# Performance work log

Hardware: AMD Instinct MI355X
Metric: run time of the kernel (lower is better)

Reference implementation:

```python
import jax, jax.numpy as jnp
import numpy as np
from jax import lax

B, T, DIN = 512, 96, 64
H = 256          # hidden_dim
P = 2            # patch_size
L = 4            # n_layers
HEADS = 8
E = 3 * H        # encoder_dim = hidden_dim * len(scales)
NC = 100         # num_classes
EPS = 1e-5


def layernorm(x, g, b):
    m = x.mean(-1, keepdims=True)
    v = ((x - m) ** 2).mean(-1, keepdims=True)
    return (x - m) * lax.rsqrt(v + EPS) * g + b


def conv1d(x, w, b, k):
    # x: [B, C, T], w: [O, I, k]; torch padding='same' (extra pad on the right for even k)
    lo = (k - 1) // 2
    hi = (k - 1) - lo
    y = lax.conv_general_dilated(x, w, (1,), [(lo, hi)],
                                 dimension_numbers=('NCH', 'OIH', 'NCH'))
    return y + b[None, :, None]


def fourier_attn(x, Wqkv, Wo, bo):
    Bx, Tx, Ex = x.shape
    dh = Ex // HEADS
    qkv = x @ Wqkv                                   # [B,T,3E]
    q, k, v = jnp.split(qkv, 3, axis=-1)
    to_heads = lambda t: t.reshape(Bx, Tx, HEADS, dh).transpose(0, 2, 1, 3)  # [B,h,T,dh]
    q, k, v = to_heads(q), to_heads(k), to_heads(v)
    qf = jnp.fft.rfft(q, axis=-2)
    kf = jnp.fft.rfft(k, axis=-2)
    attn = jnp.sum(jnp.conj(qf) * kf, axis=-1).real * (dh ** -0.5)  # [B,h,F]
    attn = jax.nn.softmax(attn, axis=-1)
    vf = jnp.fft.rfft(v, axis=-2)                    # [B,h,F,dh]
    out = jnp.fft.irfft(attn[..., None] * vf, n=Tx, axis=-2)        # [B,h,T,dh]
    out = out.transpose(0, 2, 1, 3).reshape(Bx, Tx, Ex)
    return out @ Wo + bo


def setup_inputs() -> dict:
    key = jax.random.key(0)
    ks = iter(jax.random.split(key, 40))
    nrm = lambda shape, s=0.02: jax.random.normal(next(ks), shape, jnp.float32) * s
    z = lambda *shape: jnp.zeros(shape, jnp.float32)
    o = lambda *shape: jnp.ones(shape, jnp.float32)
    return dict(
        x=jax.random.normal(next(ks), (B, T, DIN), jnp.float32),
        W_in=nrm((DIN, H)), b_in=z(H),
        pe=nrm((1, 100, H)),
        W_shape=nrm((H, H)), b_shape=z(H),
        W_patch=nrm((P * H, H)), b_patch=z(H),
        conv_w1=nrm((H, H, 1)), conv_b1=z(H),
        conv_w2=nrm((H, H, 2)), conv_b2=z(H),
        conv_w4=nrm((H, H, 4)), conv_b4=z(H),
        ln1_g=o(L, E), ln1_b=z(L, E),
        Wqkv=nrm((L, E, 3 * E)),
        Wo=nrm((L, E, E)), bo=z(L, E),
        ln2_g=o(L, E), ln2_b=z(L, E),
        Wf1=nrm((L, E, 4 * E)), bf1=z(L, 4 * E),
        Wf2=nrm((L, 4 * E, E)), bf2=z(L, E),
        ssm_w=nrm((E, E, 3)), ssm_b=z(E),
        ssm_g=o(E), ssm_bn=z(E),
        W_out=nrm((E, NC)), b_out=z(NC),
    )


def reference(x, W_in, b_in, pe, W_shape, b_shape, W_patch, b_patch,
              conv_w1, conv_b1, conv_w2, conv_b2, conv_w4, conv_b4,
              ln1_g, ln1_b, Wqkv, Wo, bo, ln2_g, ln2_b, Wf1, bf1, Wf2, bf2,
              ssm_w, ssm_b, ssm_g, ssm_bn, W_out, b_out):
    h = x @ W_in + b_in                              # [B,T,H]
    h = h + pe[:, :h.shape[1], :]
    # shape-aware embedding: diff with prepend of first step
    sf = jnp.diff(h, axis=1, prepend=h[:, :1, :])
    h = h + sf @ W_shape + b_shape
    # patch embedding: [B,T,H] -> [B,T/P,P*H] -> [B,T/P,H]
    Bx, Tx, Dx = h.shape
    h = h.reshape(Bx, Tx // P, P * Dx) @ W_patch + b_patch
    # multiscale fourier: rfft.real then 3 same-padded convs, concat channels
    f = jnp.fft.rfft(h, axis=1).real                 # [B,F,H], F = T/P//2 + 1
    fc = f.transpose(0, 2, 1)                        # [B,H,F]
    m1 = conv1d(fc, conv_w1, conv_b1, 1).transpose(0, 2, 1)
    m2 = conv1d(fc, conv_w2, conv_b2, 2).transpose(0, 2, 1)
    m4 = conv1d(fc, conv_w4, conv_b4, 4).transpose(0, 2, 1)
    h = jnp.concatenate([m1, m2, m4], axis=-1)       # [B,F,E]
    for i in range(L):
        h = h + fourier_attn(layernorm(h, ln1_g[i], ln1_b[i]), Wqkv[i], Wo[i], bo[i])
        y = layernorm(h, ln2_g[i], ln2_b[i])
        y = jax.nn.gelu(y @ Wf1[i] + bf1[i], approximate=False) @ Wf2[i] + bf2[i]
        h = h + y
    # simple SSM: depth conv residual + layernorm
    s = conv1d(h.transpose(0, 2, 1), ssm_w, ssm_b, 3).transpose(0, 2, 1)
    h = layernorm(h + s, ssm_g, ssm_bn)
    return h.mean(axis=1) @ W_out + b_out            # [B,NC]
```

## Files before the change

kernel.cpp:

```cpp
#include <hip/hip_runtime.h>
#include <hip/hip_bf16.h>
#include <math.h>

#define Bsz 512
#define Tin 96
#define DIN 64
#define Hd  256
#define Pp  2
#define Ll  4
#define NHEAD 8
#define Ed  768
#define NCls 100
#define Tp  48
#define Ff  25
#define F2  13
#define DH  96

#define E_BIAS 1
#define E_PE   2
#define E_RES  4
#define E_ACC  8
#define E_GELU 16
#define E_OUTS 32
#define E_SPLK 64

typedef unsigned short ushortT;
typedef unsigned short ushort8 __attribute__((ext_vector_type(8)));
typedef short short8 __attribute__((ext_vector_type(8)));
typedef float f32x4 __attribute__((ext_vector_type(4)));

static __device__ __forceinline__ ushortT f2bf(float f) {
  __hip_bfloat16 h = __float2bfloat16(f);
  return *reinterpret_cast<ushortT*>(&h);
}
static __device__ __forceinline__ float bfbits2f(ushortT u) {
  unsigned int x = ((unsigned int)u) << 16;
  return __uint_as_float(x);
}
static __device__ __forceinline__ void split2(float v, ushortT& h, ushortT& l) {
  h = f2bf(v);
  l = f2bf(v - bfbits2f(h));
}

typedef const __attribute__((address_space(1))) void* gas1_t;
typedef __attribute__((address_space(3))) void* las3_t;
static __device__ __forceinline__ void gload16(const void* g, void* l) {
  __builtin_amdgcn_global_load_lds((gas1_t)g, (las3_t)l, 16, 0, 0);
}

constexpr int GBM = 128, GBN = 128, GBK = 32;

template<int AMODE, int ASRC, int EPI>
__global__ __launch_bounds__(256) void gemm3(
    const float* __restrict__ A,
    const ushortT* __restrict__ Ah, const ushortT* __restrict__ Al,
    const ushortT* __restrict__ Bh, const ushortT* __restrict__ Bl,
    const float* __restrict__ bias, const float* __restrict__ extra,
    float* __restrict__ C, ushortT* __restrict__ Coh, ushortT* __restrict__ Col,
    int M, int N, int K, int Ald, int Tdim, int lo, int Kin, int Cld, int coff,
    int Mt, int Nt, int mmaj, int ksn)
{
  __shared__ __align__(16) ushortT Ash[GBM * GBK];
  __shared__ __align__(16) ushortT Asl[GBM * GBK];
  __shared__ __align__(16) ushortT Bsh[GBN * GBK];
  __shared__ __align__(16) ushortT Bsl[GBN * GBK];
  int tid = threadIdx.x;

  int lin = blockIdx.x;
  int G = gridDim.x;
  int r8 = lin & 7, s8 = lin >> 3;
  int q = G >> 3, rem = G & 7;
  int start = r8 * q + (r8 < rem ? r8 : rem);
  int idx = start + s8;
  int tiles = Mt * Nt;
  int ks = 0;
  if (ksn > 1) { ks = idx / tiles; idx -= ks * tiles; }
  int mt, nt;
  if (mmaj) { mt = idx / Nt; nt = idx - mt * Nt; }
  else      { nt = idx / Mt; mt = idx - nt * Mt; }
  int m0 = mt * GBM, n0 = nt * GBN;
  int kper = K / ksn;
  int kbeg = ks * kper, kend = kbeg + kper;

  int wid = tid >> 6, lane = tid & 63;
  int wm = wid & 1, wn = wid >> 1;
  int m16 = lane & 15, quad = lane >> 4;

  f32x4 acc[4][4] = {};

  int grow = (wid << 5) + (lane >> 2);
  int gcb  = (lane & 3) << 4;
  int scb  = gcb ^ (((grow >> 1) & 3) << 4);
  char* ldsA = (char*)Ash + (wid << 11);
  char* ldsa = (char*)Asl + (wid << 11);
  char* ldsB = (char*)Bsh + (wid << 11);
  char* ldsb = (char*)Bsl + (wid << 11);
  size_t bo0 = ((size_t)(n0 + grow) * K) * 2 + scb;
  size_t bo1 = bo0 + (size_t)(16 * K) * 2;
  size_t ao0 = 0, ao1 = 0;
  if (ASRC == 1) {
    int ar0 = m0 + grow;       if (ar0 >= M) ar0 = M - 1;
    int ar1 = m0 + grow + 16;  if (ar1 >= M) ar1 = M - 1;
    ao0 = ((size_t)ar0 * Ald) * 2 + scb;
    ao1 = ((size_t)ar1 * Ald) * 2 + scb;
  }

  int srow = tid >> 1;
  int skh  = (tid & 1) << 4;
  int sswz = ((srow >> 1) & 3) << 3;
  int st0 = srow * GBK + (skh ^ sswz);
  int st1 = srow * GBK + ((skh + 8) ^ sswz);

  int fswz = ((m16 >> 1) & 3) << 3;
  int scf  = (quad << 3) ^ fswz;

  for (int k0 = kbeg; k0 < kend; k0 += GBK) {
    size_t kb = (size_t)k0 * 2;
    gload16((const char*)Bh + bo0 + kb, ldsB);
    gload16((const char*)Bh + bo1 + kb, ldsB + 1024);
    gload16((const char*)Bl + bo0 + kb, ldsb);
    gload16((const char*)Bl + bo1 + kb, ldsb + 1024);
    if (ASRC == 1) {
      gload16((const char*)Ah + ao0 + kb, ldsA);
      gload16((const char*)Ah + ao1 + kb, ldsA + 1024);
      gload16((const char*)Al + ao0 + kb, ldsa);
      gload16((const char*)Al + ao1 + kb, ldsa + 1024);
    } else {
      int row = m0 + srow;
      if (row >= M) row = M - 1;
      float tf[16];
      if (AMODE == 0) {
        const float* p = A + (size_t)row * Ald + k0 + skh;
#pragma unroll
        for (int j = 0; j < 16; j += 4) {
          float4 v = *(const float4*)(p + j);
          tf[j] = v.x; tf[j+1] = v.y; tf[j+2] = v.z; tf[j+3] = v.w;
        }
      } else if (AMODE == 1) {
        int t = row % Tdim;
        const float* p = A + (size_t)row * Ald + k0 + skh;
#pragma unroll
        for (int j = 0; j < 16; j += 4) {
          float4 v = *(const float4*)(p + j);
          float4 w = (t != 0) ? *(const float4*)(p - Ald + j) : v;
          tf[j] = v.x - w.x; tf[j+1] = v.y - w.y;
          tf[j+2] = v.z - w.z; tf[j+3] = v.w - w.w;
        }
      } else {
        int kk = k0 + skh;
        int tap = kk / Kin;
        int i0  = kk - tap * Kin;
        int bb = row / Tdim;
        int t  = row - bb * Tdim;
        int tt = t - lo + tap;
        if (tt >= 0 && tt < Tdim) {
          const float* p = A + ((size_t)bb * Tdim + tt) * Ald + i0;
#pragma unroll
          for (int j = 0; j < 16; j += 4) {
            float4 v = *(const float4*)(p + j);
            tf[j] = v.x; tf[j+1] = v.y; tf[j+2] = v.z; tf[j+3] = v.w;
          }
        } else {
#pragma unroll
          for (int j = 0; j < 16; j++) tf[j] = 0.0f;
        }
      }
      ushortT th[16], tl[16];
#pragma unroll
      for (int j = 0; j < 16; j++) split2(tf[j], th[j], tl[j]);
      *(ushort8*)&Ash[st0] = *(ushort8*)&th[0];
      *(ushort8*)&Ash[st1] = *(ushort8*)&th[8];
      *(ushort8*)&Asl[st0] = *(ushort8*)&tl[0];
      *(ushort8*)&Asl[st1] = *(ushort8*)&tl[8];
    }
    __syncthreads();
    short8 ah[4], al[4], bh[4], bl[4];
#pragma unroll
    for (int i = 0; i < 4; i++) {
      int ro = (wm * 64 + i * 16 + m16) * GBK + scf;
      ah[i] = *(short8*)&Ash[ro];
      al[i] = *(short8*)&Asl[ro];
    }
#pragma unroll
    for (int j = 0; j < 4; j++) {
      int ro = (wn * 64 + j * 16 + m16) * GBK + scf;
      bh[j] = *(short8*)&Bsh[ro];
      bl[j] = *(short8*)&Bsl[ro];
    }
#pragma unroll
    for (int i = 0; i < 4; i++)
#pragma unroll
      for (int j = 0; j < 4; j++) {
        acc[i][j] = __builtin_amdgcn_mfma_f32_16x16x32_bf16(ah[i], bh[j], acc[i][j], 0, 0, 0);
        acc[i][j] = __builtin_amdgcn_mfma_f32_16x16x32_bf16(al[i], bh[j], acc[i][j], 0, 0, 0);
        acc[i][j] = __builtin_amdgcn_mfma_f32_16x16x32_bf16(ah[i], bl[j], acc[i][j], 0, 0, 0);
      }
    __syncthreads();
  }

#pragma unroll
  for (int i = 0; i < 4; i++) {
#pragma unroll
    for (int j = 0; j < 4; j++) {
      int colg = n0 + wn * 64 + j * 16 + m16;
#pragma unroll
      for (int rr = 0; rr < 4; rr++) {
        int rowg = m0 + wm * 64 + i * 16 + quad * 4 + rr;
        if (rowg >= M) continue;
        float v = acc[i][j][rr];
        if ((EPI & E_BIAS) && ks == 0) v += bias[colg];
        if (EPI & E_PE)   v += extra[(size_t)(rowg % Tdim) * N + colg];
        if (EPI & E_RES)  v += extra[(size_t)rowg * Cld + colg];
        if (EPI & E_GELU) v = 0.5f * v * (1.0f + erff(v * 0.70710678118654752f));
        size_t off = (size_t)rowg * Cld + coff + colg;
        if (EPI & E_SPLK) {
          atomicAdd(&C[off], v);
        } else if (EPI & E_OUTS) {
          ushortT h, l; split2(v, h, l);
          Coh[off] = h; Col[off] = l;
        } else {
          if (EPI & E_ACC) v += C[off];
          C[off] = v;
        }
      }
    }
  }
}

#define GEMM3(AM, AS, EP, KS, Asrc, AhP, AlP, BhP, BlP, biasP, extraP, CP, CohP, ColP, \
              Mv, Nv, Kv, AldV, TdimV, loV, KinV, CldV, coffV) \
  do { int Mt_ = (Mv) / GBM, Nt_ = (Nv) / GBN; int mm_ = ((Mv) >= (Nv)) ? 1 : 0; \
       gemm3<AM, AS, EP><<<dim3(Mt_ * Nt_ * (KS)), dim3(256), 0, stream>>>( \
           Asrc, AhP, AlP, BhP, BlP, biasP, extraP, CP, CohP, ColP, \
           Mv, Nv, Kv, AldV, TdimV, loV, KinV, CldV, coffV, Mt_, Nt_, mm_, KS); } while (0)

__global__ __launch_bounds__(256) void wcvt_t_split(
    const float* __restrict__ W, ushortT* __restrict__ Wh, ushortT* __restrict__ Wl,
    int K, int N)
{
  __shared__ float t[32][33];
  int k0 = blockIdx.y * 32, n0 = blockIdx.x * 32;
  int tx = threadIdx.x;
  int ty = threadIdx.y;
#pragma unroll
  for (int dy = 0; dy < 32; dy += 8)
    t[ty + dy][tx] = W[(size_t)(k0 + ty + dy) * N + n0 + tx];
  __syncthreads();
#pragma unroll
  for (int dy = 0; dy < 32; dy += 8) {
    float v = t[tx][ty + dy];
    ushortT h, l;
    split2(v, h, l);
    size_t off = (size_t)(n0 + ty + dy) * K + k0 + tx;
    Wh[off] = h; Wl[off] = l;
  }
}

__global__ __launch_bounds__(256) void wcvt_split(
    const float* __restrict__ W, ushortT* __restrict__ Wh, ushortT* __restrict__ Wl, int n)
{
  int gid = blockIdx.x * 256 + threadIdx.x;
  int stride = gridDim.x * 256;
  for (int i = gid; i < n; i += stride) {
    ushortT h, l;
    split2(W[i], h, l);
    Wh[i] = h; Wl[i] = l;
  }
}

__global__ __launch_bounds__(256) void wcvt_split_tm(
    const float* __restrict__ W, ushortT* __restrict__ Wh, ushortT* __restrict__ Wl,
    int O, int Kin, int NT)
{
  int n = O * Kin * NT;
  int gid = blockIdx.x * 256 + threadIdx.x;
  int stride = gridDim.x * 256;
  for (int idx = gid; idx < n; idx += stride) {
    int o = idx / (Kin * NT);
    int rr = idx - o * (Kin * NT);
    int tap = rr / Kin;
    int i = rr - tap * Kin;
    float v = W[(size_t)o * Kin * NT + (size_t)i * NT + tap];
    ushortT h, l;
    split2(v, h, l);
    Wh[idx] = h; Wl[idx] = l;
  }
}

constexpr int BM = 64, BN = 64, BK = 16, TM = 4, TN = 4;
__global__ __launch_bounds__(256) void gemm_cls(
    const float* __restrict__ A, const float* __restrict__ Bw,
    const float* __restrict__ bias, float* __restrict__ C,
    int M, int N, int K, int Ald, int Cld)
{
  __shared__ alignas(16) float As[BK][BM + 4];
  __shared__ alignas(16) float Bs[BK][BN + 4];
  int tid = threadIdx.x;
  int n0 = blockIdx.x * BN;
  int m0 = blockIdx.y * BM;
  int tx = tid & 15, ty = tid >> 4;
  float acc[TM][TN];
#pragma unroll
  for (int i = 0; i < TM; i++)
#pragma unroll
    for (int j = 0; j < TN; j++) acc[i][j] = 0.0f;
  int a_m = tid >> 2, a_k = (tid & 3) * 4;
  int b_k = tid >> 4, b_n = (tid & 15) * 4;
  for (int k0 = 0; k0 < K; k0 += BK) {
    int row = m0 + a_m;
#pragma unroll
    for (int j = 0; j < 4; j++)
      As[a_k + j][a_m] = A[(size_t)row * Ald + k0 + a_k + j];
    int kk = k0 + b_k;
#pragma unroll
    for (int j = 0; j < 4; j++) {
      int nn = n0 + b_n + j;
      Bs[b_k][b_n + j] = (nn < N) ? Bw[(size_t)kk * N + nn] : 0.0f;
    }
    __syncthreads();
#pragma unroll
    for (int k = 0; k < BK; k++) {
      float4 av = *reinterpret_cast<const float4*>(&As[k][ty * TM]);
      float4 bv = *reinterpret_cast<const float4*>(&Bs[k][tx * TN]);
      float a4[4] = {av.x, av.y, av.z, av.w};
      float b4[4] = {bv.x, bv.y, bv.z, bv.w};
#pragma unroll
      for (int i = 0; i < TM; i++)
#pragma unroll
        for (int j = 0; j < TN; j++) acc[i][j] += a4[i] * b4[j];
    }
    __syncthreads();
  }
#pragma unroll
  for (int i = 0; i < TM; i++) {
    int row = m0 + ty * TM + i;
#pragma unroll
    for (int j = 0; j < TN; j++) {
      int col = n0 + tx * TN + j;
      if (col >= N) continue;
      C[(size_t)row * Cld + col] = acc[i][j] + bias[col];
    }
  }
}

__global__ __launch_bounds__(256) void rfft48_kernel(
    const float* __restrict__ hp, float* __restrict__ f)
{
  int kf = blockIdx.x;
  int b  = blockIdx.y;
  int tid = threadIdx.x;
  __shared__ float ct[48];
  if (tid < 48) {
    int rr = (kf * tid) % 48;
    ct[tid] = cosf(6.2831853071795864f * (float)rr / 48.0f);
  }
  __syncthreads();
  const float* hb = hp + (size_t)b * Tp * Hd;
  float s = 0.0f;
  for (int t = 0; t < 48; t++) s += hb[t * Hd + tid] * ct[t];
  f[((size_t)b * Ff + kf) * Hd + tid] = s;
}

__global__ __launch_bounds__(256) void attn_fused(
    const float* __restrict__ qkv,
    ushortT* __restrict__ oh, ushortT* __restrict__ ol)
{
  int bh = blockIdx.x;
  int b = bh >> 3, h = bh & 7;
  __shared__ float qs[Ff * DH], ks[Ff * DH], vs[Ff * DH];
  __shared__ float ct[F2 * Ff], st[F2 * Ff];
  __shared__ float red[F2 * DH];
  __shared__ float sm[F2];
  __shared__ float G[Ff];
  int tid = threadIdx.x;
  const float* base = qkv + (size_t)b * Ff * (3 * Ed) + h * DH;
  for (int e = tid; e < Ff * DH; e += 256) {
    int t = e / DH, d = e - t * DH;
    size_t ro = (size_t)t * (3 * Ed) + d;
    qs[e] = base[ro];
    ks[e] = base[ro + Ed];
    vs[e] = base[ro + 2 * Ed];
  }
  for (int e = tid; e < F2 * Ff; e += 256) {
    int fq = e / Ff, t = e - fq * Ff;
    int rr = (fq * t) % Ff;
    float ang = 6.2831853071795864f * (float)rr / 25.0f;
    ct[e] = cosf(ang); st[e] = sinf(ang);
  }
  __syncthreads();
  for (int e = tid; e < F2 * DH; e += 256) {
    int fq = e / DH, d = e - fq * DH;
    float qr = 0, qi = 0, kr = 0, ki = 0;
    for (int t = 0; t < Ff; t++) {
      float c = ct[fq * Ff + t], s = st[fq * Ff + t];
      float qv = qs[t * DH + d], kv = ks[t * DH + d];
      qr += qv * c; qi += qv * s; kr += kv * c; ki += kv * s;
    }
    red[e] = qr * kr + qi * ki;
  }
  __syncthreads();
  if (tid < F2) {
    float s = 0;
    for (int d = 0; d < DH; d++) s += red[tid * DH + d];
    sm[tid] = s * 0.10206207261596575f;
  }
  __syncthreads();
  if (tid == 0) {
    float mx = sm[0];
    for (int f = 1; f < F2; f++) mx = fmaxf(mx, sm[f]);
    float den = 0;
    for (int f = 0; f < F2; f++) { float e2 = expf(sm[f] - mx); sm[f] = e2; den += e2; }
    float inv = 1.0f / den;
    for (int f = 0; f < F2; f++)
      sm[f] *= inv * ((f == 0) ? (1.0f / 25.0f) : (2.0f / 25.0f));
  }
  __syncthreads();
  if (tid < Ff) {
    float g = 0;
    for (int f = 0; f < F2; f++) g += sm[f] * ct[f * Ff + tid];
    G[tid] = g;
  }
  __syncthreads();
  size_t ob = ((size_t)b * Ff) * Ed + h * DH;
  for (int e = tid; e < Ff * DH; e += 256) {
    int t = e / DH, d = e - t * DH;
    float o = 0;
    int dd = t;
    for (int tp = 0; tp < Ff; tp++) {
      o += G[dd] * vs[tp * DH + d];
      dd--; if (dd < 0) dd += Ff;
    }
    ushortT hh, ll;
    split2(o, hh, ll);
    size_t off = ob + (size_t)t * Ed + d;
    oh[off] = hh; ol[off] = ll;
  }
}

__global__ __launch_bounds__(256) void ln_split(
    const float* __restrict__ x, const float* __restrict__ g,
    const float* __restrict__ bb, ushortT* __restrict__ yh, ushortT* __restrict__ yl)
{
  int row = blockIdx.x;
  int tid = threadIdx.x;
  const float* xr = x + (size_t)row * Ed;
  float v0 = xr[tid], v1 = xr[tid + 256], v2 = xr[tid + 512];
  __shared__ float rs[256];
  rs[tid] = v0 + v1 + v2;
  __syncthreads();
  for (int o = 128; o > 0; o >>= 1) {
    if (tid < o) rs[tid] += rs[tid + o];
    __syncthreads();
  }
  float m = rs[0] * (1.0f / 768.0f);
  __syncthreads();
  float d0 = v0 - m, d1 = v1 - m, d2 = v2 - m;
  rs[tid] = d0 * d0 + d1 * d1 + d2 * d2;
  __syncthreads();
  for (int o = 128; o > 0; o >>= 1) {
    if (tid < o) rs[tid] += rs[tid + o];
    __syncthreads();
  }
  float inv = rsqrtf(rs[0] * (1.0f / 768.0f) + 1e-5f);
  size_t basei = (size_t)row * Ed;
  float o0 = d0 * inv * g[tid] + bb[tid];
  float o1 = d1 * inv * g[tid + 256] + bb[tid + 256];
  float o2 = d2 * inv * g[tid + 512] + bb[tid + 512];
  ushortT h, l;
  split2(o0, h, l); yh[basei + tid] = h;       yl[basei + tid] = l;
  split2(o1, h, l); yh[basei + tid + 256] = h; yl[basei + tid + 256] = l;
  split2(o2, h, l); yh[basei + tid + 512] = h; yl[basei + tid + 512] = l;
}

__global__ __launch_bounds__(256) void ln_f32(
    const float* __restrict__ x, const float* __restrict__ g,
    const float* __restrict__ bb, float* __restrict__ y)
{
  int row = blockIdx.x;
  int tid = threadIdx.x;
  const float* xr = x + (size_t)row * Ed;
  float v0 = xr[tid], v1 = xr[tid + 256], v2 = xr[tid + 512];
  __shared__ float rs[256];
  rs[tid] = v0 + v1 + v2;
  __syncthreads();
  for (int o = 128; o > 0; o >>= 1) {
    if (tid < o) rs[tid] += rs[tid + o];
    __syncthreads();
  }
  float m = rs[0] * (1.0f / 768.0f);
  __syncthreads();
  float d0 = v0 - m, d1 = v1 - m, d2 = v2 - m;
  rs[tid] = d0 * d0 + d1 * d1 + d2 * d2;
  __syncthreads();
  for (int o = 128; o > 0; o >>= 1) {
    if (tid < o) rs[tid] += rs[tid + o];
    __syncthreads();
  }
  float inv = rsqrtf(rs[0] * (1.0f / 768.0f) + 1e-5f);
  float* yr = y + (size_t)row * Ed;
  yr[tid]       = d0 * inv * g[tid]       + bb[tid];
  yr[tid + 256] = d1 * inv * g[tid + 256] + bb[tid + 256];
  yr[tid + 512] = d2 * inv * g[tid + 512] + bb[tid + 512];
}

__global__ __launch_bounds__(256) void mean_kernel(
    const float* __restrict__ x, float* __restrict__ y)
{
  int b = blockIdx.x;
  int tid = threadIdx.x;
  for (int c = tid; c < Ed; c += 256) {
    float s = 0;
    for (int t = 0; t < Ff; t++) s += x[((size_t)b * Ff + t) * Ed + c];
    y[(size_t)b * Ed + c] = s * (1.0f / 25.0f);
  }
}

extern "C" void kernel_launch(void* const* d_in, const int* in_sizes, int n_in,
                              void* d_out, int out_size, void* d_ws, size_t ws_size,
                              hipStream_t stream)
{
  const float* x       = (const float*)d_in[0];
  const float* W_in    = (const float*)d_in[1];
  const float* b_in    = (const float*)d_in[2];
  const float* pe      = (const float*)d_in[3];
  const float* W_shape = (const float*)d_in[4];
  const float* b_shape = (const float*)d_in[5];
  const float* W_patch = (const float*)d_in[6];
  const float* b_patch = (const float*)d_in[7];
  const float* conv_w1 = (const float*)d_in[8];
  const float* conv_b1 = (const float*)d_in[9];
  const float* conv_w2 = (const float*)d_in[10];
  const float* conv_b2 = (const float*)d_in[11];
  const float* conv_w4 = (const float*)d_in[12];
  const float* conv_b4 = (const float*)d_in[13];
  const float* ln1_g   = (const float*)d_in[14];
  const float* ln1_b   = (const float*)d_in[15];
  const float* Wqkv    = (const float*)d_in[16];
  const float* Wo      = (const float*)d_in[17];
  const float* bo      = (const float*)d_in[18];
  const float* ln2_g   = (const float*)d_in[19];
  const float* ln2_b   = (const float*)d_in[20];
  const float* Wf1     = (const float*)d_in[21];
  const float* bf1     = (const float*)d_in[22];
  const float* Wf2     = (const float*)d_in[23];
  const float* bf2     = (const float*)d_in[24];
  const float* ssm_w   = (const float*)d_in[25];
  const float* ssm_b   = (const float*)d_in[26];
  const float* ssm_g   = (const float*)d_in[27];
  const float* ssm_bn  = (const float*)d_in[28];
  const float* W_out   = (const float*)d_in[29];
  const float* b_out   = (const float*)d_in[30];
  float* out = (float*)d_out;

  float* hbuf = (float*)d_ws;
  ushortT* Ahp = (ushortT*)(hbuf + 9830400);
  ushortT* Alp = Ahp + 9830400;
  float* pool = (float*)(Alp + 9830400);

  dim3 blk(256);
  dim3 wblk(32, 8);
  const int Mf = Bsz * Ff;
  const ushortT* NUS = nullptr;
  const float* NF = nullptr;
  ushortT* NU = nullptr;

  ushortT* p0w = (ushortT*)(pool + 6291456);
  ushortT* WinH = p0w + 0;        ushortT* WinL = p0w + 16384;
  ushortT* WshH = p0w + 32768;    ushortT* WshL = p0w + 98304;
  ushortT* WpaH = p0w + 163840;   ushortT* WpaL = p0w + 294912;
  ushortT* c1H  = p0w + 425984;   ushortT* c1L  = p0w + 491520;
  ushortT* c2H  = p0w + 557056;   ushortT* c2L  = p0w + 688128;
  ushortT* c4H  = p0w + 819200;   ushortT* c4L  = p0w + 1081344;
  wcvt_t_split<<<dim3(Hd / 32, DIN / 32), wblk, 0, stream>>>(W_in, WinH, WinL, DIN, Hd);
  wcvt_t_split<<<dim3(Hd / 32, Hd / 32), wblk, 0, stream>>>(W_shape, WshH, WshL, Hd, Hd);
  wcvt_t_split<<<dim3(Hd / 32, (Pp * Hd) / 32), wblk, 0, stream>>>(W_patch, WpaH, WpaL, Pp * Hd, Hd);
  wcvt_split<<<64, blk, 0, stream>>>(conv_w1, c1H, c1L, Hd * Hd);
  wcvt_split_tm<<<128, blk, 0, stream>>>(conv_w2, c2H, c2L, Hd, Hd, 2);
  wcvt_split_tm<<<256, blk, 0, stream>>>(conv_w4, c4H, c4L, Hd, Hd, 4);

  float* s0 = (float*)Ahp;
  float* s1 = pool;
  for (int c = 0; c < 2; c++) {
    const int NB = 256;
    const int M96 = NB * Tin;
    const int Mpch = NB * Tp;
    const int Mfch = NB * Ff;
    const float* xc = x + (size_t)c * NB * Tin * DIN;

    GEMM3(0, 0, E_BIAS | E_PE, 1, xc, NUS, NUS, WinH, WinL, b_in, pe, s0, NU, NU,
          M96, Hd, DIN, DIN, Tin, 0, 0, Hd, 0);
    GEMM3(1, 0, E_BIAS | E_RES, 1, s0, NUS, NUS, WshH, WshL, b_shape, s0, s1, NU, NU,
          M96, Hd, Hd, Hd, Tin, 0, 0, Hd, 0);
    GEMM3(0, 0, E_BIAS, 1, s1, NUS, NUS, WpaH, WpaL, b_patch, NF, s0, NU, NU,
          Mpch, Hd, Pp * Hd, Pp * Hd, 0, 0, 0, Hd, 0);
    rfft48_kernel<<<dim3(Ff, NB), blk, 0, stream>>>(s0, s1);
    float* hrows = hbuf + (size_t)c * Mfch * Ed;
    GEMM3(0, 0, E_BIAS, 1, s1, NUS, NUS, c1H, c1L, conv_b1, NF, hrows, NU, NU,
          Mfch, Hd, Hd, Hd, Ff, 0, 0, Ed, 0);
    GEMM3(2, 0, E_BIAS, 1, s1, NUS, NUS, c2H, c2L, conv_b2, NF, hrows, NU, NU,
          Mfch, Hd, Hd * 2, Hd, Ff, 0, Hd, Ed, Hd);
    GEMM3(2, 0, E_BIAS, 1, s1, NUS, NUS, c4H, c4L, conv_b4, NF, hrows, NU, NU,
          Mfch, Hd, Hd * 4, Hd, Ff, 1, Hd, Ed, 2 * Hd);
  }

  float* qkvbuf = pool;
  ushortT* lwA = (ushortT*)(pool + 7372800);
  ushortT* qkH = lwA + 0;        ushortT* qkL = lwA + 1769472;
  ushortT* woH = lwA + 3538944;  ushortT* woL = lwA + 4128768;
  ushortT* Ch2 = (ushortT*)pool;
  ushortT* Cl2 = Ch2 + 6291456;
  ushortT* lwB = (ushortT*)(pool + 6291456);
  ushortT* f1H = lwB + 0;        ushortT* f1L = lwB + 2359296;
  ushortT* f2H = lwB + 4718592;  ushortT* f2L = lwB + 7077888;

  const int NBA = 128;
  const int Mca = NBA * Ff;

  for (int l = 0; l < Ll; l++) {
    const float* Wqkv_l = Wqkv + (size_t)l * Ed * (3 * Ed);
    const float* Wo_l   = Wo   + (size_t)l * Ed * Ed;
    const float* bo_l   = bo   + (size_t)l * Ed;
    const float* Wf1_l  = Wf1  + (size_t)l * Ed * (4 * Ed);
    const float* bf1_l  = bf1  + (size_t)l * (4 * Ed);
    const float* Wf2_l  = Wf2  + (size_t)l * (4 * Ed) * Ed;
    const float* bf2_l  = bf2  + (size_t)l * Ed;

    wcvt_t_split<<<dim3((3 * Ed) / 32, Ed / 32), wblk, 0, stream>>>(Wqkv_l, qkH, qkL, Ed, 3 * Ed);
    wcvt_t_split<<<dim3(Ed / 32, Ed / 32), wblk, 0, stream>>>(Wo_l, woH, woL, Ed, Ed);

    ln_split<<<Mf, blk, 0, stream>>>(hbuf, ln1_g + (size_t)l * Ed, ln1_b + (size_t)l * Ed, Ahp, Alp);

    for (int c = 0; c < 4; c++) {
      ushortT* ah = Ahp + (size_t)c * Mca * Ed;
      ushortT* al = Alp + (size_t)c * Mca * Ed;
      GEMM3(0, 1, 0, 1, NF, ah, al, qkH, qkL, NF, NF, qkvbuf, NU, NU,
            Mca, 3 * Ed, Ed, Ed, 0, 0, 0, 3 * Ed, 0);
      attn_fused<<<NBA * NHEAD, blk, 0, stream>>>(qkvbuf, ah, al);
    }
    GEMM3(0, 1, E_BIAS | E_ACC, 1, NF, Ahp, Alp, woH, woL, bo_l, NF, hbuf, NU, NU,
          Mf, Ed, Ed, Ed, 0, 0, 0, Ed, 0);

    wcvt_t_split<<<dim3((4 * Ed) / 32, Ed / 32), wblk, 0, stream>>>(Wf1_l, f1H, f1L, Ed, 4 * Ed);
    wcvt_t_split<<<dim3(Ed / 32, (4 * Ed) / 32), wblk, 0, stream>>>(Wf2_l, f2H, f2L, 4 * Ed, Ed);

    ln_split<<<Mf, blk, 0, stream>>>(hbuf, ln2_g + (size_t)l * Ed, ln2_b + (size_t)l * Ed, Ahp, Alp);

    for (int row0 = 0; row0 < Mf; row0 += 2048) {
      int rows = (Mf - row0 < 2048) ? (Mf - row0) : 2048;
      GEMM3(0, 1, E_BIAS | E_GELU | E_OUTS, 1, NF,
            Ahp + (size_t)row0 * Ed, Alp + (size_t)row0 * Ed, f1H, f1L, bf1_l, NF,
            (float*)nullptr, Ch2, Cl2, rows, 4 * Ed, Ed, Ed, 0, 0, 0, 4 * Ed, 0);
      GEMM3(0, 1, E_BIAS | E_SPLK, 4, NF, Ch2, Cl2, f2H, f2L, bf2_l, NF,
            hbuf + (size_t)row0 * Ed, NU, NU, rows, Ed, 4 * Ed, 4 * Ed, 0, 0, 0, Ed, 0);
    }
  }

  ushortT* ssH = (ushortT*)pool; ushortT* ssL = ssH + 1769472;
  wcvt_split_tm<<<512, blk, 0, stream>>>(ssm_w, ssH, ssL, Ed, Ed, 3);
  float* S = (float*)Ahp;
  GEMM3(2, 0, E_BIAS | E_RES, 1, hbuf, NUS, NUS, ssH, ssL, ssm_b, hbuf, S, NU, NU,
        Mf, Ed, Ed * 3, Ed, Ff, 1, Ed, Ed, 0);

  float* L = pool;
  ln_f32<<<Mf, blk, 0, stream>>>(S, ssm_g, ssm_bn, L);
  float* mout = (float*)Ahp;
  mean_kernel<<<Bsz, blk, 0, stream>>>(L, mout);
  gemm_cls<<<dim3(2, Bsz / BM), blk, 0, stream>>>(
      mout, W_out, b_out, out, Bsz, NCls, Ed, Ed, NCls);
}
```

Baseline: 5.899 ms.

## Double-buffer GEMM LDS tiles to overlap global loads with MFMA compute

The shared GEMM kernel now keeps two LDS buffers for the A and B hi/lo tiles. It issues the global-to-LDS loads for the next K step before computing the current one, and ends each iteration with one explicit waitcnt and barrier instead of two syncthreads. It also raises wave priority around the MFMA block. The aim is to hide global load latency behind matrix math, at the cost of doubling LDS use to 64KB per block, which may lower occupancy.

```diff
diff --git a/kernel.cpp b/kernel.cpp
--- a/kernel.cpp
+++ b/kernel.cpp
@@ -60,10 +60,10 @@
     int M, int N, int K, int Ald, int Tdim, int lo, int Kin, int Cld, int coff,
     int Mt, int Nt, int mmaj, int ksn)
 {
-  __shared__ __align__(16) ushortT Ash[GBM * GBK];
-  __shared__ __align__(16) ushortT Asl[GBM * GBK];
-  __shared__ __align__(16) ushortT Bsh[GBN * GBK];
-  __shared__ __align__(16) ushortT Bsl[GBN * GBK];
+  __shared__ __align__(16) ushortT Ash[2][GBM * GBK];
+  __shared__ __align__(16) ushortT Asl[2][GBM * GBK];
+  __shared__ __align__(16) ushortT Bsh[2][GBN * GBK];
+  __shared__ __align__(16) ushortT Bsl[2][GBN * GBK];
   int tid = threadIdx.x;
 
   int lin = blockIdx.x;
@@ -91,10 +91,6 @@
   int grow = (wid << 5) + (lane >> 2);
   int gcb  = (lane & 3) << 4;
   int scb  = gcb ^ (((grow >> 1) & 3) << 4);
-  char* ldsA = (char*)Ash + (wid << 11);
-  char* ldsa = (char*)Asl + (wid << 11);
-  char* ldsB = (char*)Bsh + (wid << 11);
-  char* ldsb = (char*)Bsl + (wid << 11);
   size_t bo0 = ((size_t)(n0 + grow) * K) * 2 + scb;
   size_t bo1 = bo0 + (size_t)(16 * K) * 2;
   size_t ao0 = 0, ao1 = 0;
@@ -114,13 +110,19 @@
   int fswz = ((m16 >> 1) & 3) << 3;
   int scf  = (quad << 3) ^ fswz;
 
-  for (int k0 = kbeg; k0 < kend; k0 += GBK) {
+  auto stage = [&](int bsel, int k0) {
     size_t kb = (size_t)k0 * 2;
-    gload16((const char*)Bh + bo0 + kb, ldsB);
-    gload16((const char*)Bh + bo1 + kb, ldsB + 1024);
-    gload16((const char*)Bl + bo0 + kb, ldsb);
-    gload16((const char*)Bl + bo1 + kb, ldsb + 1024);
+    {
+      char* ldsB = (char*)&Bsh[bsel][0] + (wid << 11);
+      char* ldsb = (char*)&Bsl[bsel][0] + (wid << 11);
+      gload16((const char*)Bh + bo0 + kb, ldsB);
+      gload16((const char*)Bh + bo1 + kb, ldsB + 1024);
+      gload16((const char*)Bl + bo0 + kb, ldsb);
+      gload16((const char*)Bl + bo1 + kb, ldsb + 1024);
+    }
     if (ASRC == 1) {
+      char* ldsA = (char*)&Ash[bsel][0] + (wid << 11);
+      char* ldsa = (char*)&Asl[bsel][0] + (wid << 11);
       gload16((const char*)Ah + ao0 + kb, ldsA);
       gload16((const char*)Ah + ao1 + kb, ldsA + 1024);
       gload16((const char*)Al + ao0 + kb, ldsa);
@@ -168,25 +170,38 @@
       ushortT th[16], tl[16];
 #pragma unroll
       for (int j = 0; j < 16; j++) split2(tf[j], th[j], tl[j]);
-      *(ushort8*)&Ash[st0] = *(ushort8*)&th[0];
-      *(ushort8*)&Ash[st1] = *(ushort8*)&th[8];
-      *(ushort8*)&Asl[st0] = *(ushort8*)&tl[0];
-      *(ushort8*)&Asl[st1] = *(ushort8*)&tl[8];
-    }
-    __syncthreads();
+      *(ushort8*)&Ash[bsel][st0] = *(ushort8*)&th[0];
+      *(ushort8*)&Ash[bsel][st1] = *(ushort8*)&th[8];
+      *(ushort8*)&Asl[bsel][st0] = *(ushort8*)&tl[0];
+      *(ushort8*)&Asl[bsel][st1] = *(ushort8*)&tl[8];
+    }
+  };
+
+  int nsteps = (kend - kbeg) / GBK;
+
+  stage(0, kbeg);
+  asm volatile("s_waitcnt vmcnt(0) lgkmcnt(0)" ::: "memory");
+  __builtin_amdgcn_s_barrier();
+
+  int cur = 0;
+  for (int s = 0; s < nsteps; ++s) {
+    if (s + 1 < nsteps) stage(cur ^ 1, kbeg + (s + 1) * GBK);
+
     short8 ah[4], al[4], bh[4], bl[4];
 #pragma unroll
     for (int i = 0; i < 4; i++) {
       int ro = (wm * 64 + i * 16 + m16) * GBK + scf;
-      ah[i] = *(short8*)&Ash[ro];
-      al[i] = *(short8*)&Asl[ro];
+      ah[i] = *(short8*)&Ash[cur][ro];
+      al[i] = *(short8*)&Asl[cur][ro];
     }
 #pragma unroll
     for (int j = 0; j < 4; j++) {
       int ro = (wn * 64 + j * 16 + m16) * GBK + scf;
-      bh[j] = *(short8*)&Bsh[ro];
-      bl[j] = *(short8*)&Bsl[ro];
-    }
+      bh[j] = *(short8*)&Bsh[cur][ro];
+      bl[j] = *(short8*)&Bsl[cur][ro];
+    }
+
+    __builtin_amdgcn_s_setprio(1);
 #pragma unroll
     for (int i = 0; i < 4; i++)
 #pragma unroll
@@ -195,7 +210,11 @@
         acc[i][j] = __builtin_amdgcn_mfma_f32_16x16x32_bf16(al[i], bh[j], acc[i][j], 0, 0, 0);
         acc[i][j] = __builtin_amdgcn_mfma_f32_16x16x32_bf16(ah[i], bl[j], acc[i][j], 0, 0, 0);
       }
-    __syncthreads();
+    __builtin_amdgcn_s_setprio(0);
+
+    asm volatile("s_waitcnt vmcnt(0) lgkmcnt(0)" ::: "memory");
+    __builtin_amdgcn_s_barrier();
+    cur ^= 1;
   }
 
 #pragma unroll
```

Result: no change. 5.997 ms (+1.7%).
